# Optimization experiments

Measured on AMD Instinct MI355X. Metric: run time of the kernel, lower is better.

## Reference

```python
import jax, jax.numpy as jnp
import numpy as np

EMBED = 1024
B, I, J = 8, 2048, 2048
SCALE = EMBED ** -0.5


def setup_inputs() -> dict:
    key = jax.random.key(0)
    ks = jax.random.split(key, 5)
    s = EMBED ** -0.5  # init scale for weights
    return {
        "q_in": jax.random.normal(ks[0], (B, I, EMBED), dtype=jnp.float32),
        "k_v": jax.random.normal(ks[1], (B, J, EMBED), dtype=jnp.float32),
        "Wq": jax.random.normal(ks[2], (EMBED, EMBED), dtype=jnp.float32) * s,
        "bq": jnp.zeros((EMBED,), dtype=jnp.float32),
        "Wk": jax.random.normal(ks[3], (EMBED, EMBED), dtype=jnp.float32) * s,
        "bk": jnp.zeros((EMBED,), dtype=jnp.float32),
        "Wv": jax.random.normal(ks[4], (EMBED, EMBED), dtype=jnp.float32) * s,
        "bv": jnp.zeros((EMBED,), dtype=jnp.float32),
    }


def reference(q_in, k_v, Wq, bq, Wk, bk, Wv, bv):
    # Linear projections (torch Linear: x @ W.T + b; here W stored as [in, out])
    q = q_in @ Wq + bq            # [b, i, d]
    k = k_v @ Wk + bk             # [b, j, d]
    v = k_v @ Wv + bv             # [b, j, d]
    sim = jnp.einsum('bid,bjd->bij', q, k) * SCALE  # [b, i, j]
    attn = jax.nn.softmax(sim, axis=-1)
    # dropout with drop_rate=0.0 is identity
    out = jnp.einsum('bij,bjd->bid', attn, v)       # [b, i, d]
    return out
```

## Files before the change

kernel.cpp:

```cpp
#include <hip/hip_runtime.h>
#include <hip/hip_bf16.h>


#define BATCH 8
#define SEQ   2048
#define EMB   1024
#define SC2   0.045084222f

typedef __attribute__((ext_vector_type(8))) short bf16x8;
typedef __attribute__((ext_vector_type(4))) float f32x4;
typedef __attribute__((ext_vector_type(4))) unsigned short u16x4;
typedef __attribute__((ext_vector_type(8))) unsigned short u16x8;
typedef __attribute__((ext_vector_type(4))) float fl4;

__device__ __forceinline__ unsigned short f2bf(float f) {
    unsigned u = __builtin_bit_cast(unsigned, f);
    unsigned r = u + 0x7fffu + ((u >> 16) & 1u);
    return (unsigned short)(r >> 16);
}
__device__ __forceinline__ float bf2f(unsigned short s) {
    return __builtin_bit_cast(float, ((unsigned)s) << 16);
}
__device__ __forceinline__ void gload16(const unsigned short* g, unsigned short* l) {
    __builtin_amdgcn_global_load_lds(
        (const __attribute__((address_space(1))) void*)g,
        (__attribute__((address_space(3))) void*)l, 16, 0, 0);
}

__global__ __launch_bounds__(256)
void convert_in(const float* __restrict__ q_in, const float* __restrict__ k_v,
                unsigned short* __restrict__ qbin, unsigned short* __restrict__ kvbin)
{
    const size_t N = (size_t)BATCH * SEQ * EMB;
    size_t idx = ((size_t)blockIdx.x * 256 + threadIdx.x) * 8;
    const size_t stride = (size_t)gridDim.x * 256 * 8;
    for (; idx < N; idx += stride) {
        fl4 a0 = *(const fl4*)&q_in[idx];
        fl4 a1 = *(const fl4*)&q_in[idx + 4];
        fl4 b0 = *(const fl4*)&k_v[idx];
        fl4 b1 = *(const fl4*)&k_v[idx + 4];
        u16x8 ua, ub;
#pragma unroll
        for (int i = 0; i < 4; i++) {
            ua[i] = f2bf(a0[i]); ua[i + 4] = f2bf(a1[i]);
            ub[i] = f2bf(b0[i]); ub[i + 4] = f2bf(b1[i]);
        }
        *(u16x8*)&qbin[idx] = ua;
        *(u16x8*)&kvbin[idx] = ub;
    }
}

__global__ __launch_bounds__(256)
void convert_w(const float* __restrict__ Wq, const float* __restrict__ Wk,
               const float* __restrict__ Wv, unsigned short* __restrict__ Wt)
{
    const int wsel = blockIdx.y;
    const float* W = (wsel == 0) ? Wq : (wsel == 1) ? Wk : Wv;
    unsigned short* O = Wt + (size_t)wsel * EMB * EMB;
    const int k0 = (blockIdx.x >> 4) * 64;
    const int n0 = (blockIdx.x & 15) * 64;
    __shared__ unsigned short l[64 * 65];
    const int tid = threadIdx.x;
#pragma unroll
    for (int it = 0; it < 16; it++) {
        const int lin = it * 256 + tid;
        const int k = lin >> 6, n = lin & 63;
        l[n * 65 + k] = f2bf(W[(size_t)(k0 + k) * EMB + n0 + n]);
    }
    __syncthreads();
#pragma unroll
    for (int it = 0; it < 16; it++) {
        const int lin = it * 256 + tid;
        const int n = lin >> 6, k = lin & 63;
        O[(size_t)(n0 + n) * EMB + k0 + k] = l[n * 65 + k];
    }
}

__device__ __forceinline__ void stageT(const unsigned short* lanebase, size_t rstride,
                                       unsigned short* lwave) {
#pragma unroll
    for (int i = 0; i < 2; i++)
        gload16(lanebase + (size_t)(i * 128) * rstride, lwave + i * 4096);
}

#define PIPE_PHASE1(SLOT, DO_STAGE, STAGE_A_BASE, STAGE_A_LDS)                  \
    {                                                                           \
        const unsigned short* pa = &sA[SLOT][0];                                \
        const unsigned short* pb = &sB[SLOT][0];                                \
        bf16x8 a0 = *(bf16x8*)&pa[aoff0];                                       \
        bf16x8 a1 = *(bf16x8*)&pa[aoff0 + 512];                                 \
        bf16x8 a2 = *(bf16x8*)&pa[aoff0 + 1024];                                \
        bf16x8 a3 = *(bf16x8*)&pa[aoff0 + 1536];                                \
        bv0 = *(bf16x8*)&pb[boff0];                                             \
        bv1 = *(bf16x8*)&pb[boff0 + 512];                                       \
        bv2 = *(bf16x8*)&pb[boff0 + 1024];                                      \
        bv3 = *(bf16x8*)&pb[boff0 + 1536];                                      \
        if (DO_STAGE) stageT(STAGE_A_BASE, strideA, STAGE_A_LDS);               \
        __builtin_amdgcn_s_barrier();                                           \
        asm volatile("s_waitcnt lgkmcnt(0)" ::: "memory");                      \
        __builtin_amdgcn_sched_barrier(0);                                      \
        __builtin_amdgcn_s_setprio(1);                                          \
        acc[0][0] = __builtin_amdgcn_mfma_f32_16x16x32_bf16(a0, bv0, acc[0][0], 0, 0, 0); \
        acc[0][1] = __builtin_amdgcn_mfma_f32_16x16x32_bf16(a0, bv1, acc[0][1], 0, 0, 0); \
        acc[0][2] = __builtin_amdgcn_mfma_f32_16x16x32_bf16(a0, bv2, acc[0][2], 0, 0, 0); \
        acc[0][3] = __builtin_amdgcn_mfma_f32_16x16x32_bf16(a0, bv3, acc[0][3], 0, 0, 0); \
        acc[1][0] = __builtin_amdgcn_mfma_f32_16x16x32_bf16(a1, bv0, acc[1][0], 0, 0, 0); \
        acc[1][1] = __builtin_amdgcn_mfma_f32_16x16x32_bf16(a1, bv1, acc[1][1], 0, 0, 0); \
        acc[1][2] = __builtin_amdgcn_mfma_f32_16x16x32_bf16(a1, bv2, acc[1][2], 0, 0, 0); \
        acc[1][3] = __builtin_amdgcn_mfma_f32_16x16x32_bf16(a1, bv3, acc[1][3], 0, 0, 0); \
        acc[2][0] = __builtin_amdgcn_mfma_f32_16x16x32_bf16(a2, bv0, acc[2][0], 0, 0, 0); \
        acc[2][1] = __builtin_amdgcn_mfma_f32_16x16x32_bf16(a2, bv1, acc[2][1], 0, 0, 0); \
        acc[2][2] = __builtin_amdgcn_mfma_f32_16x16x32_bf16(a2, bv2, acc[2][2], 0, 0, 0); \
        acc[2][3] = __builtin_amdgcn_mfma_f32_16x16x32_bf16(a2, bv3, acc[2][3], 0, 0, 0); \
        acc[3][0] = __builtin_amdgcn_mfma_f32_16x16x32_bf16(a3, bv0, acc[3][0], 0, 0, 0); \
        acc[3][1] = __builtin_amdgcn_mfma_f32_16x16x32_bf16(a3, bv1, acc[3][1], 0, 0, 0); \
        acc[3][2] = __builtin_amdgcn_mfma_f32_16x16x32_bf16(a3, bv2, acc[3][2], 0, 0, 0); \
        acc[3][3] = __builtin_amdgcn_mfma_f32_16x16x32_bf16(a3, bv3, acc[3][3], 0, 0, 0); \
        __builtin_amdgcn_s_setprio(0);                                          \
        __builtin_amdgcn_s_barrier();                                           \
        __builtin_amdgcn_sched_barrier(0);                                      \
    }

#define PIPE_PHASE2(SLOT, DO_STAGE, STAGE_B_BASE, STAGE_B_LDS)                  \
    {                                                                           \
        const unsigned short* pa = &sA[SLOT][0];                                \
        bf16x8 a0 = *(bf16x8*)&pa[aoff0 + 2048];                                \
        bf16x8 a1 = *(bf16x8*)&pa[aoff0 + 2560];                                \
        bf16x8 a2 = *(bf16x8*)&pa[aoff0 + 3072];                                \
        bf16x8 a3 = *(bf16x8*)&pa[aoff0 + 3584];                                \
        if (DO_STAGE) stageT(STAGE_B_BASE, strideB, STAGE_B_LDS);               \
        __builtin_amdgcn_s_barrier();                                           \
        asm volatile("s_waitcnt lgkmcnt(0)" ::: "memory");                      \
        __builtin_amdgcn_sched_barrier(0);                                      \
        __builtin_amdgcn_s_setprio(1);                                          \
        acc[4][0] = __builtin_amdgcn_mfma_f32_16x16x32_bf16(a0, bv0, acc[4][0], 0, 0, 0); \
        acc[4][1] = __builtin_amdgcn_mfma_f32_16x16x32_bf16(a0, bv1, acc[4][1], 0, 0, 0); \
        acc[4][2] = __builtin_amdgcn_mfma_f32_16x16x32_bf16(a0, bv2, acc[4][2], 0, 0, 0); \
        acc[4][3] = __builtin_amdgcn_mfma_f32_16x16x32_bf16(a0, bv3, acc[4][3], 0, 0, 0); \
        acc[5][0] = __builtin_amdgcn_mfma_f32_16x16x32_bf16(a1, bv0, acc[5][0], 0, 0, 0); \
        acc[5][1] = __builtin_amdgcn_mfma_f32_16x16x32_bf16(a1, bv1, acc[5][1], 0, 0, 0); \
        acc[5][2] = __builtin_amdgcn_mfma_f32_16x16x32_bf16(a1, bv2, acc[5][2], 0, 0, 0); \
        acc[5][3] = __builtin_amdgcn_mfma_f32_16x16x32_bf16(a1, bv3, acc[5][3], 0, 0, 0); \
        acc[6][0] = __builtin_amdgcn_mfma_f32_16x16x32_bf16(a2, bv0, acc[6][0], 0, 0, 0); \
        acc[6][1] = __builtin_amdgcn_mfma_f32_16x16x32_bf16(a2, bv1, acc[6][1], 0, 0, 0); \
        acc[6][2] = __builtin_amdgcn_mfma_f32_16x16x32_bf16(a2, bv2, acc[6][2], 0, 0, 0); \
        acc[6][3] = __builtin_amdgcn_mfma_f32_16x16x32_bf16(a2, bv3, acc[6][3], 0, 0, 0); \
        acc[7][0] = __builtin_amdgcn_mfma_f32_16x16x32_bf16(a3, bv0, acc[7][0], 0, 0, 0); \
        acc[7][1] = __builtin_amdgcn_mfma_f32_16x16x32_bf16(a3, bv1, acc[7][1], 0, 0, 0); \
        acc[7][2] = __builtin_amdgcn_mfma_f32_16x16x32_bf16(a3, bv2, acc[7][2], 0, 0, 0); \
        acc[7][3] = __builtin_amdgcn_mfma_f32_16x16x32_bf16(a3, bv3, acc[7][3], 0, 0, 0); \
        __builtin_amdgcn_s_setprio(0);                                          \
        asm volatile("s_waitcnt vmcnt(4)" ::: "memory");                        \
        __builtin_amdgcn_s_barrier();                                           \
        __builtin_amdgcn_sched_barrier(0);                                      \
    }

__device__ __forceinline__ void pipe_gemm(
    const unsigned short* __restrict__ Asrc,
    const unsigned short* __restrict__ Bsrc,
    const size_t strideA, const size_t strideB, const int NT,
    unsigned short (*sA)[8192], unsigned short (*sB)[8192],
    const int lwave, const int aoff0, const int boff0,
    f32x4 acc[8][4])
{
    stageT(Asrc, strideA, &sA[0][lwave]);
    stageT(Bsrc, strideB, &sB[0][lwave]);
    stageT(Asrc + 32, strideA, &sA[1][lwave]);
    stageT(Bsrc + 32, strideB, &sB[1][lwave]);
    asm volatile("s_waitcnt vmcnt(4)" ::: "memory");
    __builtin_amdgcn_s_barrier();
    __builtin_amdgcn_sched_barrier(0);

    bf16x8 bv0, bv1, bv2, bv3;
    for (int T = 0; T < NT; ++T) {
        const int s = T & 3;
        const int doStage = (T + 2 < NT);
        const int s2 = (T + 2) & 3;
        PIPE_PHASE1(s, doStage, Asrc + (T + 2) * 32, &sA[s2][lwave]);
        PIPE_PHASE2(s, doStage, Bsrc + (T + 2) * 32, &sB[s2][lwave]);
    }
}

#define PIPE_PREAMBLE                                                     \
    __shared__ unsigned short sA[4][8192];                                \
    __shared__ unsigned short sB[4][8192];                                \
    const int tid = threadIdx.x, lane = tid & 63;                         \
    const int wid = tid >> 6, wr = wid >> 2, wn = wid & 3;                \
    const int r = lane & 15, g = lane >> 4;                               \
    const int lwave = (wid << 9);                                         \
    const int aoff0 = (wr * 128 + r) * 32 + g * 8;                        \
    const int boff0 = (wn * 64 + r) * 32 + g * 8;                         \
    f32x4 acc[8][4];                                                      \
    _Pragma("unroll") for (int i_ = 0; i_ < 8; i_++)                      \
    _Pragma("unroll") for (int j_ = 0; j_ < 4; j_++) acc[i_][j_] = (f32x4)0.0f;

__global__ __launch_bounds__(512, 1)
void proj_q256(const unsigned short* __restrict__ Wqt,
               const unsigned short* __restrict__ X,
               const float* __restrict__ bias,
               unsigned short* __restrict__ qb)
{
    PIPE_PREAMBLE
    const int bid = blockIdx.x;
    const int lid = (bid & 7) * 32 + (bid >> 3);
    const int dt = lid & 3, it = lid >> 2;
    const int d0 = dt * 256, i0 = it * 256;
    const size_t strideA = EMB, strideB = EMB;
    const unsigned short* Asrc = Wqt + (size_t)(d0 + (tid >> 2)) * EMB + (tid & 3) * 8;
    const unsigned short* Bsrc = X + (size_t)(i0 + (tid >> 2)) * EMB + (tid & 3) * 8;

    pipe_gemm(Asrc, Bsrc, strideA, strideB, EMB / 32, sA, sB, lwave, aoff0, boff0, acc);

#pragma unroll
    for (int mm = 0; mm < 8; mm++) {
        const int dbase = d0 + wr * 128 + mm * 16 + g * 4;
        const fl4 b4 = *(const fl4*)&bias[dbase];
#pragma unroll
        for (int n = 0; n < 4; n++) {
            const int i = i0 + wn * 64 + n * 16 + r;
            u16x4 u;
#pragma unroll
            for (int c = 0; c < 4; c++) u[c] = f2bf(acc[mm][n][c] + b4[c]);
            *(u16x4*)&qb[(size_t)i * EMB + dbase] = u;
        }
    }
}

__global__ __launch_bounds__(512, 1)
void proj_kv256(const unsigned short* __restrict__ X,
                const unsigned short* __restrict__ Wkvt,
                const float* __restrict__ bk, const float* __restrict__ bv,
                unsigned short* __restrict__ kb, unsigned short* __restrict__ vt)
{
    PIPE_PREAMBLE
    const int bid = blockIdx.x;
    const int lid = (bid & 7) * 64 + (bid >> 3);
    const int nt = lid & 7, mt = lid >> 3;
    const int m0 = mt * 256, n0 = nt * 256;
    const size_t strideA = EMB, strideB = EMB;
    const unsigned short* Asrc = X + (size_t)(m0 + (tid >> 2)) * EMB + (tid & 3) * 8;
    const unsigned short* Bsrc = Wkvt + (size_t)(n0 + (tid >> 2)) * EMB + (tid & 3) * 8;

    pipe_gemm(Asrc, Bsrc, strideA, strideB, EMB / 32, sA, sB, lwave, aoff0, boff0, acc);

    const int b = m0 >> 11;
    const int j0l = m0 & 2047;
    if (n0 < 1024) {
#pragma unroll
        for (int mm = 0; mm < 8; mm++) {
            const int ibase = m0 + wr * 128 + mm * 16 + g * 4;
#pragma unroll
            for (int n = 0; n < 4; n++) {
                const int col = n0 + wn * 64 + n * 16 + r;
                const float bb = bk[col];
#pragma unroll
                for (int c = 0; c < 4; c++)
                    kb[(size_t)(ibase + c) * EMB + col] = f2bf(acc[mm][n][c] + bb);
            }
        }
    } else {
#pragma unroll
        for (int mm = 0; mm < 8; mm++) {
            const int jbase = j0l + wr * 128 + mm * 16 + g * 4;
#pragma unroll
            for (int n = 0; n < 4; n++) {
                const int d = n0 - 1024 + wn * 64 + n * 16 + r;
                const float bb = bv[d];
                u16x4 u;
#pragma unroll
                for (int c = 0; c < 4; c++) u[c] = f2bf(acc[mm][n][c] + bb);
                *(u16x4*)&vt[((size_t)b * EMB + d) * SEQ + jbase] = u;
            }
        }
    }
}

__global__ __launch_bounds__(512, 1)
void qk256_kernel(const unsigned short* __restrict__ qb,
                  const unsigned short* __restrict__ kb,
                  unsigned short* __restrict__ P,
                  float* __restrict__ Ppart)
{
    PIPE_PREAMBLE
    const int bid = blockIdx.x;
    const int lid = (bid & 7) * 64 + (bid >> 3);
    const int b = lid >> 6, jt = (lid >> 3) & 7, it = lid & 7;
    const int j0 = jt * 256, i0 = it * 256;
    const size_t strideA = EMB, strideB = EMB;
    const unsigned short* Ag = kb + (size_t)b * SEQ * EMB;
    const unsigned short* Bg = qb + (size_t)b * SEQ * EMB;
    const unsigned short* Asrc = Ag + (size_t)(j0 + (tid >> 2)) * EMB + (tid & 3) * 8;
    const unsigned short* Bsrc = Bg + (size_t)(i0 + (tid >> 2)) * EMB + (tid & 3) * 8;

    pipe_gemm(Asrc, Bsrc, strideA, strideB, EMB / 32, sA, sB, lwave, aoff0, boff0, acc);

    unsigned short* Pb = P + (size_t)b * SEQ * SEQ;
    float ps[4] = {0.f, 0.f, 0.f, 0.f};
#pragma unroll
    for (int mm = 0; mm < 8; mm++) {
        const int jbase = j0 + wr * 128 + mm * 16 + g * 4;
#pragma unroll
        for (int n = 0; n < 4; n++) {
            const int i = i0 + wn * 64 + n * 16 + r;
            u16x4 u;
#pragma unroll
            for (int c = 0; c < 4; c++) {
                const float p = exp2f(acc[mm][n][c] * SC2);
                ps[n] += p;
                u[c] = f2bf(p);
            }
            *(u16x4*)&Pb[(size_t)i * SEQ + jbase] = u;
        }
    }
#pragma unroll
    for (int n = 0; n < 4; n++) {
        ps[n] += __shfl_xor(ps[n], 16);
        ps[n] += __shfl_xor(ps[n], 32);
    }
    if (g == 0) {
        const int slot = jt * 2 + wr;
        float* pp = Ppart + (size_t)slot * (BATCH * SEQ) + (size_t)b * SEQ;
#pragma unroll
        for (int n = 0; n < 4; n++)
            pp[i0 + wn * 64 + n * 16 + r] = ps[n];
    }
}

__global__ __launch_bounds__(256)
void rowsum_final(const float* __restrict__ Ppart, float* __restrict__ rs)
{
    const int row = blockIdx.x * 256 + threadIdx.x;
    float s = 0.f;
#pragma unroll
    for (int slot = 0; slot < 16; slot++)
        s += Ppart[(size_t)slot * (BATCH * SEQ) + row];
    rs[row] = s;
}

__global__ __launch_bounds__(512, 1)
void pv256_kernel(const unsigned short* __restrict__ P,
                  const unsigned short* __restrict__ vt,
                  const float* __restrict__ rs,
                  float* __restrict__ out)
{
    PIPE_PREAMBLE
    const int bid = blockIdx.x;
    const int lid = (bid & 7) * 32 + (bid >> 3);
    const int b = lid >> 5, it = (lid >> 2) & 7, dt = lid & 3;
    const int d0 = dt * 256, i0 = it * 256;
    const size_t strideA = SEQ, strideB = SEQ;
    const unsigned short* Ag = vt + (size_t)b * EMB * SEQ;
    const unsigned short* Bg = P + (size_t)b * SEQ * SEQ;
    const unsigned short* Asrc = Ag + (size_t)(d0 + (tid >> 2)) * SEQ + (tid & 3) * 8;
    const unsigned short* Bsrc = Bg + (size_t)(i0 + (tid >> 2)) * SEQ + (tid & 3) * 8;

    pipe_gemm(Asrc, Bsrc, strideA, strideB, SEQ / 32, sA, sB, lwave, aoff0, boff0, acc);

    float* ob = out + (size_t)b * SEQ * EMB;
    const float* rsb = rs + (size_t)b * SEQ;
    float inv[4];
#pragma unroll
    for (int n = 0; n < 4; n++)
        inv[n] = 1.0f / rsb[i0 + wn * 64 + n * 16 + r];
#pragma unroll
    for (int mm = 0; mm < 8; mm++) {
        const int dbase = d0 + wr * 128 + mm * 16 + g * 4;
#pragma unroll
        for (int n = 0; n < 4; n++) {
            const int i = i0 + wn * 64 + n * 16 + r;
            fl4 o;
#pragma unroll
            for (int c = 0; c < 4; c++) o[c] = acc[mm][n][c] * inv[n];
            *(fl4*)&ob[(size_t)i * EMB + dbase] = o;
        }
    }
}

extern "C" void kernel_launch(void* const* d_in, const int* in_sizes, int n_in,
                              void* d_out, int out_size, void* d_ws, size_t ws_size,
                              hipStream_t stream)
{
    const float* q_in = (const float*)d_in[0];
    const float* k_v  = (const float*)d_in[1];
    const float* Wq   = (const float*)d_in[2];
    const float* bq   = (const float*)d_in[3];
    const float* Wk   = (const float*)d_in[4];
    const float* bk   = (const float*)d_in[5];
    const float* Wv   = (const float*)d_in[6];
    const float* bv   = (const float*)d_in[7];
    float* out = (float*)d_out;

    char* ws = (char*)d_ws;
    unsigned short* qbin = (unsigned short*)(ws);
    unsigned short* kvbin= (unsigned short*)(ws + (size_t)33554432);
    unsigned short* P    = (unsigned short*)(ws);
    unsigned short* qb   = (unsigned short*)(ws + (size_t)67108864);
    unsigned short* kb   = (unsigned short*)(ws + (size_t)100663296);
    unsigned short* vt   = (unsigned short*)(ws + (size_t)134217728);
    unsigned short* Wt   = (unsigned short*)(ws + (size_t)167772160);
    float*          Ppart= (float*)(ws + (size_t)174063616);
    float*          rs   = (float*)(ws + (size_t)175112192);

    convert_in<<<4096, 256, 0, stream>>>(q_in, k_v, qbin, kvbin);
    convert_w<<<dim3(256, 3), 256, 0, stream>>>(Wq, Wk, Wv, Wt);
    proj_q256<<<256, 512, 0, stream>>>(Wt, qbin, bq, qb);
    proj_kv256<<<512, 512, 0, stream>>>(kvbin, Wt + (size_t)EMB * EMB, bk, bv, kb, vt);
    qk256_kernel<<<512, 512, 0, stream>>>(qb, kb, P, Ppart);
    rowsum_final<<<64, 256, 0, stream>>>(Ppart, rs);
    pv256_kernel<<<256, 512, 0, stream>>>(P, vt, rs, out);
}
```

Before: 323.6 us.

## Stage GEMM epilogue outputs through swizzled LDS for coalesced global stores

Each GEMM kernel (Q projection, V-transposed projection, QK/exp, PV) now writes its accumulator tile into a swizzled shared-memory buffer reused from the pipeline staging area. After a barrier, a flush loop writes full 512-byte rows to global memory with 16-byte stores. This replaces the scattered 8-byte column-strided stores. The PV kernel handles its fp32 tile in two halves to fit in LDS. The cost is extra barriers and LDS traffic in the epilogue.

```diff
diff --git a/kernel.cpp b/kernel.cpp
--- a/kernel.cpp
+++ b/kernel.cpp
@@ -182,8 +182,9 @@
 }
 
 #define PIPE_PREAMBLE                                                     \
-    __shared__ unsigned short sA[4][8192];                                \
-    __shared__ unsigned short sB[4][8192];                                \
+    __shared__ unsigned short sMem[65536];                    \
+    unsigned short (*sA)[8192] = (unsigned short (*)[8192])sMem;          \
+    unsigned short (*sB)[8192] = (unsigned short (*)[8192])(sMem + 32768);\
     const int tid = threadIdx.x, lane = tid & 63;                         \
     const int wid = tid >> 6, wr = wid >> 2, wn = wid & 3;                \
     const int r = lane & 15, g = lane >> 4;                               \
@@ -194,6 +195,21 @@
     _Pragma("unroll") for (int i_ = 0; i_ < 8; i_++)                      \
     _Pragma("unroll") for (int j_ = 0; j_ < 4; j_++) acc[i_][j_] = (f32x4)0.0f;
 
+__device__ __forceinline__ void lds_flush_bf16(const unsigned short* sP,
+                                               unsigned short* gbase,
+                                               size_t gstride, int tid)
+{
+    const int lane = tid & 63, wv = tid >> 6;
+    const int rowsel = lane >> 5, jj = lane & 31;
+#pragma unroll
+    for (int it = 0; it < 16; ++it) {
+        const int row = it * 16 + wv * 2 + rowsel;
+        const int byte = row * 512 + ((jj * 16) ^ ((row & 7) << 4));
+        u16x8 v = *(const u16x8*)((const char*)sP + byte);
+        *(u16x8*)&gbase[(size_t)row * gstride + jj * 8] = v;
+    }
+}
+
 __global__ __launch_bounds__(512, 1)
 void proj_q256(const unsigned short* __restrict__ Wqt,
                const unsigned short* __restrict__ X,
@@ -213,17 +229,20 @@
 
 #pragma unroll
     for (int mm = 0; mm < 8; mm++) {
-        const int dbase = d0 + wr * 128 + mm * 16 + g * 4;
-        const fl4 b4 = *(const fl4*)&bias[dbase];
+        const int colb = wr * 128 + mm * 16 + g * 4;
+        const fl4 b4 = *(const fl4*)&bias[d0 + colb];
 #pragma unroll
         for (int n = 0; n < 4; n++) {
-            const int i = i0 + wn * 64 + n * 16 + r;
+            const int row = wn * 64 + n * 16 + r;
             u16x4 u;
 #pragma unroll
             for (int c = 0; c < 4; c++) u[c] = f2bf(acc[mm][n][c] + b4[c]);
-            *(u16x4*)&qb[(size_t)i * EMB + dbase] = u;
-        }
-    }
+            const int byte = row * 512 + ((colb * 2) ^ ((row & 7) << 4));
+            *(u16x4*)((char*)sMem + byte) = u;
+        }
+    }
+    __syncthreads();
+    lds_flush_bf16(sMem, qb + (size_t)i0 * EMB + d0, EMB, tid);
 }
 
 __global__ __launch_bounds__(512, 1)
@@ -261,17 +280,21 @@
     } else {
 #pragma unroll
         for (int mm = 0; mm < 8; mm++) {
-            const int jbase = j0l + wr * 128 + mm * 16 + g * 4;
+            const int colb = wr * 128 + mm * 16 + g * 4;
 #pragma unroll
             for (int n = 0; n < 4; n++) {
-                const int d = n0 - 1024 + wn * 64 + n * 16 + r;
-                const float bb = bv[d];
+                const int row = wn * 64 + n * 16 + r;
+                const float bb = bv[n0 - 1024 + row];
                 u16x4 u;
 #pragma unroll
                 for (int c = 0; c < 4; c++) u[c] = f2bf(acc[mm][n][c] + bb);
-                *(u16x4*)&vt[((size_t)b * EMB + d) * SEQ + jbase] = u;
+                const int byte = row * 512 + ((colb * 2) ^ ((row & 7) << 4));
+                *(u16x4*)((char*)sMem + byte) = u;
             }
         }
+        __syncthreads();
+        lds_flush_bf16(sMem, vt + ((size_t)b * EMB + (n0 - 1024)) * SEQ + j0l,
+                       SEQ, tid);
     }
 }
 
@@ -294,14 +317,13 @@
 
     pipe_gemm(Asrc, Bsrc, strideA, strideB, EMB / 32, sA, sB, lwave, aoff0, boff0, acc);
 
-    unsigned short* Pb = P + (size_t)b * SEQ * SEQ;
     float ps[4] = {0.f, 0.f, 0.f, 0.f};
 #pragma unroll
     for (int mm = 0; mm < 8; mm++) {
-        const int jbase = j0 + wr * 128 + mm * 16 + g * 4;
+        const int colb = wr * 128 + mm * 16 + g * 4;
 #pragma unroll
         for (int n = 0; n < 4; n++) {
-            const int i = i0 + wn * 64 + n * 16 + r;
+            const int row = wn * 64 + n * 16 + r;
             u16x4 u;
 #pragma unroll
             for (int c = 0; c < 4; c++) {
@@ -309,7 +331,8 @@
                 ps[n] += p;
                 u[c] = f2bf(p);
             }
-            *(u16x4*)&Pb[(size_t)i * SEQ + jbase] = u;
+            const int byte = row * 512 + ((colb * 2) ^ ((row & 7) << 4));
+            *(u16x4*)((char*)sMem + byte) = u;
         }
     }
 #pragma unroll
@@ -324,6 +347,9 @@
         for (int n = 0; n < 4; n++)
             pp[i0 + wn * 64 + n * 16 + r] = ps[n];
     }
+    __syncthreads();
+    unsigned short* Pb = P + (size_t)b * SEQ * SEQ;
+    lds_flush_bf16(sMem, Pb + (size_t)i0 * SEQ + j0, SEQ, tid);
 }
 
 __global__ __launch_bounds__(256)
@@ -362,17 +388,37 @@
 #pragma unroll
     for (int n = 0; n < 4; n++)
         inv[n] = 1.0f / rsb[i0 + wn * 64 + n * 16 + r];
-#pragma unroll
-    for (int mm = 0; mm < 8; mm++) {
-        const int dbase = d0 + wr * 128 + mm * 16 + g * 4;
-#pragma unroll
-        for (int n = 0; n < 4; n++) {
-            const int i = i0 + wn * 64 + n * 16 + r;
-            fl4 o;
-#pragma unroll
-            for (int c = 0; c < 4; c++) o[c] = acc[mm][n][c] * inv[n];
-            *(fl4*)&ob[(size_t)i * EMB + dbase] = o;
-        }
+
+    float* sF = (float*)sMem;
+#pragma unroll
+    for (int h = 0; h < 2; h++) {
+        if (wr == h) {
+#pragma unroll
+            for (int mm = 0; mm < 8; mm++) {
+                const int colb = mm * 16 + g * 4;
+#pragma unroll
+                for (int n = 0; n < 4; n++) {
+                    const int row = wn * 64 + n * 16 + r;
+                    fl4 o;
+#pragma unroll
+                    for (int c = 0; c < 4; c++) o[c] = acc[mm][n][c] * inv[n];
+                    const int byte = row * 512 + ((colb * 4) ^ ((row & 7) << 4));
+                    *(fl4*)((char*)sF + byte) = o;
+                }
+            }
+        }
+        __syncthreads();
+        {
+            const int rowsel = lane >> 5, jj = lane & 31;
+#pragma unroll
+            for (int itx = 0; itx < 16; ++itx) {
+                const int row = itx * 16 + wid * 2 + rowsel;
+                const int byte = row * 512 + ((jj * 16) ^ ((row & 7) << 4));
+                fl4 v = *(const fl4*)((const char*)sF + byte);
+                *(fl4*)&ob[(size_t)(i0 + row) * EMB + d0 + h * 128 + jj * 4] = v;
+            }
+        }
+        if (h == 0) __syncthreads();
     }
 }
 
```

Result: faster. 315.2 us (-2.6%).
